# Optimization experiments

Measured on AMD Instinct MI355X. Metric: run time of the kernel, lower is better.

## Reference

```python
import jax, jax.numpy as jnp
import numpy as np

EPS = 1e-5

def _bin(t):
    # sign() with straight-through estimator (matches the .data-mutation trick)
    s = jnp.where(t >= 0, 1.0, -1.0).astype(t.dtype)
    return t + jax.lax.stop_gradient(s - t)

def _bn(x, g, b, m, v):
    # BatchNorm1d in eval mode: running mean/var
    return (x - m) * (g * jax.lax.rsqrt(v + EPS)) + b

def _hardtanh(x):
    return jnp.clip(x, -1.0, 1.0)

def setup_inputs() -> dict:
    key = jax.random.key(0)
    ks = jax.random.split(key, 24)
    B, D, H, C = 16384, 784, 768, 10
    d = {}
    d["x"] = jax.random.normal(ks[0], (B, D), jnp.float32)
    # BinarizeLinear weights (will be sign-binarized in forward) + real-valued biases
    d["W1"] = jax.random.normal(ks[1], (H, D), jnp.float32) * 0.05
    d["b1"] = jax.random.normal(ks[2], (H,), jnp.float32) * 0.05
    d["W2"] = jax.random.normal(ks[3], (H, H), jnp.float32) * 0.05
    d["b2"] = jax.random.normal(ks[4], (H,), jnp.float32) * 0.05
    d["W3"] = jax.random.normal(ks[5], (H, H), jnp.float32) * 0.05
    d["b3"] = jax.random.normal(ks[6], (H,), jnp.float32) * 0.05
    d["W4"] = jax.random.normal(ks[7], (C, H), jnp.float32) * 0.05
    d["b4"] = jax.random.normal(ks[8], (C,), jnp.float32) * 0.05
    # BatchNorm params (eval-mode running stats)
    for i, kk in zip((1, 2, 3), ((9, 10, 11, 12), (13, 14, 15, 16), (17, 18, 19, 20))):
        d[f"g{i}"] = jax.random.normal(ks[kk[0]], (H,), jnp.float32) * 0.1 + 1.0
        d[f"be{i}"] = jax.random.normal(ks[kk[1]], (H,), jnp.float32) * 0.1
        d[f"m{i}"] = jax.random.normal(ks[kk[2]], (H,), jnp.float32) * 0.1
        d[f"v{i}"] = jax.random.uniform(ks[kk[3]], (H,), jnp.float32, 0.5, 1.5)
    return d

def reference(x, W1, b1, W2, b2, W3, b3, W4, b4,
              g1, be1, m1, v1, g2, be2, m2, v2, g3, be3, m3, v3):
    x = x.reshape(-1, 784)
    # fc1: input has 784 features -> input NOT binarized; weight binarized
    h = x @ _bin(W1).T + b1
    h = _hardtanh(_bn(h, g1, be1, m1, v1))
    # fc2: input binarized, weight binarized
    h = _bin(h) @ _bin(W2).T + b2
    h = _hardtanh(_bn(h, g2, be2, m2, v2))
    # fc3 (dropout is identity in eval mode)
    h = _bin(h) @ _bin(W3).T + b3
    h = _hardtanh(_bn(h, g3, be3, m3, v3))
    # fc4: plain Linear + LogSoftmax
    logits = h @ W4.T + b4
    return jax.nn.log_softmax(logits, axis=-1)
```

## Files before the change

### kernel.cpp

```cpp
#include <hip/hip_runtime.h>
#include <math.h>
#include <stdint.h>

#define NB 16384
#define NH 768
#define ND 784
#define NC 10
#define NW 12

__global__ void k_bnprep_f32(const float* __restrict__ g, const float* __restrict__ be,
                             const float* __restrict__ m, const float* __restrict__ v,
                             const float* __restrict__ bias, float* __restrict__ out) {
    int i = blockIdx.x * 256 + threadIdx.x;
    if (i >= NH) return;
    float t1 = __fadd_rn(v[i], 1e-5f);
    float t2 = __fsqrt_rn(t1);
    float t3 = __fdiv_rn(1.0f, t2);
    out[i]          = __fmul_rn(g[i], t3);
    out[NH + i]     = m[i];
    out[2 * NH + i] = be[i];
    out[3 * NH + i] = bias[i];
}

__global__ void k_pack_w1bf(const float* __restrict__ W1, unsigned short* __restrict__ wbf) {
    int k = blockIdx.x * 256 + threadIdx.x;
    int col = blockIdx.y;
    if (k >= ND) return;
    float v = W1[(size_t)col * ND + k];
    wbf[(size_t)col * ND + k] = (v >= 0.0f) ? (unsigned short)0x3F80 : (unsigned short)0xBF80;
}

__global__ void k_pack_wT(const float* __restrict__ W, unsigned long long* __restrict__ wT) {
    int idx = blockIdx.x * 256 + threadIdx.x;
    if (idx >= NH * NW) return;
    int col = idx / NW, j = idx % NW;
    unsigned long long w = 0ull;
    for (int l = 0; l < 64; ++l) {
        float v = W[(size_t)col * NH + j * 64 + l];
        w |= (unsigned long long)(v >= 0.0f ? 1 : 0) << l;
    }
    wT[(size_t)j * NH + col] = w;
}

__global__ __launch_bounds__(512, 4)
void k_gemm1_bf(const float* __restrict__ x, const unsigned short* __restrict__ wbf,
                const float* __restrict__ bnp,
                unsigned int* __restrict__ s1p32) {
    __shared__ float xs[8][ND];
    __shared__ alignas(16) unsigned short wl[32][808];
    const int tid = threadIdx.x;
    const int r0 = blockIdx.x * 8;
    const int wave = tid >> 6, lane = tid & 63;
    const int colsub = lane & 31, jh = lane >> 5;
    const int j0 = jh * 8;

    {
        const float4* src = (const float4*)(x + (size_t)(r0 + wave) * ND);
        float4* dst = (float4*)&xs[wave][0];
        for (int k4 = lane; k4 < 196; k4 += 64) dst[k4] = src[k4];
    }

    const float* xrow = &xs[wave][j0];

#pragma unroll 1
    for (int tile = 0; tile < 2; ++tile) {
        const int c0 = blockIdx.y * 64 + tile * 32;
        __syncthreads();
        {
            int c = tid >> 4, q = tid & 15;
            uint4* dst = (uint4*)&wl[c][0];
            const uint4* srcp = (const uint4*)(wbf + (size_t)(c0 + c) * ND);
#pragma unroll
            for (int k4 = q; k4 < 98; k4 += 16) dst[k4] = srcp[k4];
        }
        __syncthreads();

        const unsigned short* wrow = &wl[colsub][j0];

        float a[4][8];
#pragma unroll
        for (int g = 0; g < 4; ++g)
#pragma unroll
            for (int i = 0; i < 8; ++i) a[g][i] = 0.0f;

#pragma unroll
        for (int t = 0; t < 12; ++t) {
#pragma unroll
            for (int g = 0; g < 4; ++g) {
                const int kk = t * 64 + g * 16;
                uint4 wA = *(const uint4*)(wrow + kk);
                float4 x0 = *(const float4*)(xrow + kk);
                float4 x1 = *(const float4*)(xrow + kk + 4);
                unsigned int dw[4] = {wA.x, wA.y, wA.z, wA.w};
                float wf[8];
#pragma unroll
                for (int p = 0; p < 4; ++p) {
                    wf[2 * p]     = __uint_as_float(dw[p] << 16);
                    wf[2 * p + 1] = __uint_as_float(dw[p] & 0xFFFF0000u);
                }
                float xv[8] = {x0.x, x0.y, x0.z, x0.w, x1.x, x1.y, x1.z, x1.w};
#pragma unroll
                for (int i = 0; i < 8; ++i)
                    a[g][i] = __fmaf_rn(wf[i], xv[i], a[g][i]);
            }
        }
        {
            const int kk = 768;
            uint4 wA = *(const uint4*)(wrow + kk);
            float4 x0 = *(const float4*)(xrow + kk);
            float4 x1 = *(const float4*)(xrow + kk + 4);
            unsigned int dw[4] = {wA.x, wA.y, wA.z, wA.w};
            float wf[8];
#pragma unroll
            for (int p = 0; p < 4; ++p) {
                wf[2 * p]     = __uint_as_float(dw[p] << 16);
                wf[2 * p + 1] = __uint_as_float(dw[p] & 0xFFFF0000u);
            }
            float xv[8] = {x0.x, x0.y, x0.z, x0.w, x1.x, x1.y, x1.z, x1.w};
#pragma unroll
            for (int i = 0; i < 8; ++i)
                a[0][i] = __fmaf_rn(wf[i], xv[i], a[0][i]);
        }

        float v[8];
#pragma unroll
        for (int i = 0; i < 8; ++i)
            v[i] = __fadd_rn(__fadd_rn(a[0][i], a[1][i]), __fadd_rn(a[2][i], a[3][i]));
        float h8[8];
#pragma unroll
        for (int i = 0; i < 8; ++i) {
            float other = __shfl_xor(v[i], 32, 64);
            h8[i] = __fadd_rn(v[i], other);
        }
        float h4[4], h2[2];
#pragma unroll
        for (int i = 0; i < 4; ++i) h4[i] = __fadd_rn(h8[i], h8[i + 4]);
#pragma unroll
        for (int i = 0; i < 2; ++i) h2[i] = __fadd_rn(h4[i], h4[i + 2]);
        float acc = __fadd_rn(h2[0], h2[1]);

        const int col = c0 + colsub;
        const float sc = bnp[col], mm = bnp[NH + col], be = bnp[2 * NH + col],
                    bias = bnp[3 * NH + col];
        float h  = __fadd_rn(acc, bias);
        float t1 = __fsub_rn(h, mm);
        float u  = __fmul_rn(t1, sc);
        float hb = __fadd_rn(u, be);
        unsigned long long word = __ballot(hb >= 0.0f);
        if (lane == 0)
            s1p32[(size_t)(r0 + wave) * (2 * NW) + blockIdx.y * 2 + tile] =
                (unsigned int)word;
    }
}

template <int MODE>
__global__ __launch_bounds__(256, 2)
void k_popbin(const unsigned long long* __restrict__ Ap,
              const unsigned long long* __restrict__ wT,
              const float* __restrict__ bnp,
              unsigned long long* __restrict__ Sp, float* __restrict__ h_out) {
    __shared__ unsigned long long as[64][NW];
    const int tid = threadIdx.x;
    const int b0 = blockIdx.x * 64;

    {
        unsigned long long* asf = &as[0][0];
        const unsigned long long* src = Ap + (size_t)b0 * NW;
        for (int i = tid; i < 64 * NW; i += 256) asf[i] = src[i];
    }
    __syncthreads();

    const int wave = tid >> 6, lane = tid & 63;

    for (int chunk = 0; chunk < NW; ++chunk) {
        const int col = chunk * 64 + lane;
        unsigned long long w[NW];
#pragma unroll
        for (int j = 0; j < NW; ++j) w[j] = wT[(size_t)j * NH + col];
        const float sc = bnp[col], mm = bnp[NH + col], be = bnp[2 * NH + col],
                    bias = bnp[3 * NH + col];
        for (int r = 0; r < 16; ++r) {
            const int row = wave * 16 + r;
            int d = 0;
#pragma unroll
            for (int j = 0; j < NW; ++j)
                d += __builtin_popcountll(as[row][j] ^ w[j]);
            int dot = NH - 2 * d;
            float h  = __fadd_rn((float)dot, bias);
            float t  = __fsub_rn(h, mm);
            float u  = __fmul_rn(t, sc);
            float hb = __fadd_rn(u, be);
            if (MODE == 0) {
                unsigned long long word = __ballot(hb >= 0.0f);
                if (lane == 0) Sp[(size_t)(b0 + row) * NW + chunk] = word;
            } else {
                float hc = fminf(fmaxf(hb, -1.0f), 1.0f);
                h_out[(size_t)(b0 + row) * NH + col] = hc;
            }
        }
    }
}

__global__ __launch_bounds__(256, 4)
void k_fc4(const float* __restrict__ h3, const float* __restrict__ W4,
           const float* __restrict__ b4, float* __restrict__ out) {
    __shared__ float w4s[NC * NH];
    const int tid = threadIdx.x;
    for (int i = tid; i < NC * NH; i += 256) w4s[i] = W4[i];
    __syncthreads();

    const int wave = tid >> 6, lane = tid & 63;
    const int row = blockIdx.x * 4 + wave;
    const float* hrow = h3 + (size_t)row * NH;

    double p[NC];
#pragma unroll
    for (int c = 0; c < NC; ++c) p[c] = 0.0;

    for (int it = 0; it < NH / 64; ++it) {
        int j = it * 64 + lane;
        double hv = (double)hrow[j];
#pragma unroll
        for (int c = 0; c < NC; ++c) p[c] += hv * (double)w4s[c * NH + j];
    }
#pragma unroll
    for (int c = 0; c < NC; ++c) {
#pragma unroll
        for (int off = 32; off > 0; off >>= 1) p[c] += __shfl_xor(p[c], off, 64);
    }
    double lg[NC];
    double mx = -1e300;
#pragma unroll
    for (int c = 0; c < NC; ++c) {
        lg[c] = p[c] + (double)b4[c];
        mx = fmax(mx, lg[c]);
    }
    double s = 0.0;
#pragma unroll
    for (int c = 0; c < NC; ++c) s += exp(lg[c] - mx);
    double lse = mx + log(s);
    if (lane < NC) {
        double v = 0.0;
#pragma unroll
        for (int c = 0; c < NC; ++c)
            if (lane == c) v = lg[c];
        out[(size_t)row * NC + lane] = (float)(v - lse);
    }
}

extern "C" void kernel_launch(void* const* d_in, const int* in_sizes, int n_in,
                              void* d_out, int out_size, void* d_ws, size_t ws_size,
                              hipStream_t stream) {
    const float* x  = (const float*)d_in[0];
    const float* W1 = (const float*)d_in[1];
    const float* b1 = (const float*)d_in[2];
    const float* W2 = (const float*)d_in[3];
    const float* b2 = (const float*)d_in[4];
    const float* W3 = (const float*)d_in[5];
    const float* b3 = (const float*)d_in[6];
    const float* W4 = (const float*)d_in[7];
    const float* b4 = (const float*)d_in[8];
    const float* g1 = (const float*)d_in[9],  *be1 = (const float*)d_in[10];
    const float* m1 = (const float*)d_in[11], *v1  = (const float*)d_in[12];
    const float* g2 = (const float*)d_in[13], *be2 = (const float*)d_in[14];
    const float* m2 = (const float*)d_in[15], *v2  = (const float*)d_in[16];
    const float* g3 = (const float*)d_in[17], *be3 = (const float*)d_in[18];
    const float* m3 = (const float*)d_in[19], *v3  = (const float*)d_in[20];
    float* out = (float*)d_out;

    char* ws = (char*)d_ws;
    size_t off = 0;
    unsigned short* wbf = (unsigned short*)(ws + off);  off += (size_t)NH * ND * 2;
    unsigned long long* w2pT = (unsigned long long*)(ws + off); off += (size_t)NW * NH * 8;
    unsigned long long* w3pT = (unsigned long long*)(ws + off); off += (size_t)NW * NH * 8;
    unsigned long long* s1p  = (unsigned long long*)(ws + off); off += (size_t)NB * NW * 8;
    unsigned long long* s2p  = (unsigned long long*)(ws + off); off += (size_t)NB * NW * 8;
    float*  h3   = (float*)(ws + off);              off += (size_t)NB * NH * 4;
    float* bnp1 = (float*)(ws + off);               off += (size_t)4 * NH * 4;
    float* bnp2 = (float*)(ws + off);               off += (size_t)4 * NH * 4;
    float* bnp3 = (float*)(ws + off);               off += (size_t)4 * NH * 4;
    (void)ws_size; (void)in_sizes; (void)n_in; (void)out_size;

    k_pack_w1bf<<<dim3(4, NH), 256, 0, stream>>>(W1, wbf);
    k_pack_wT<<<dim3((NH * NW + 255) / 256), 256, 0, stream>>>(W2, w2pT);
    k_pack_wT<<<dim3((NH * NW + 255) / 256), 256, 0, stream>>>(W3, w3pT);
    k_bnprep_f32<<<dim3(3), 256, 0, stream>>>(g1, be1, m1, v1, b1, bnp1);
    k_bnprep_f32<<<dim3(3), 256, 0, stream>>>(g2, be2, m2, v2, b2, bnp2);
    k_bnprep_f32<<<dim3(3), 256, 0, stream>>>(g3, be3, m3, v3, b3, bnp3);

    k_gemm1_bf<<<dim3(NB / 8, NH / 64), 512, 0, stream>>>(x, wbf, bnp1,
                                                          (unsigned int*)s1p);
    k_popbin<0><<<dim3(NB / 64), 256, 0, stream>>>(s1p, w2pT, bnp2, s2p, nullptr);
    k_popbin<1><<<dim3(NB / 64), 256, 0, stream>>>(s2p, w3pT, bnp3, nullptr, h3);
    k_fc4<<<dim3(NB / 4), 256, 0, stream>>>(h3, W4, b4, out);
}
```

Baseline: 883.1 us.

## Use packed FP32 FMA and compute two rows per wave in gemm1

Rewrites the first-layer kernel so each wave handles two batch rows instead of one. This halves the block to 256 threads and reuses each decoded bf16 weight pair across both rows. The inner products use inline v_pk_fma_f32, doing two FMAs per instruction and cutting the VALU instruction count and LDS weight reads per output. The cost is more accumulator registers (64 floats) and fewer threads per block for the weight tile loads, which may lower occupancy.

```diff
diff --git a/kernel.cpp b/kernel.cpp
--- a/kernel.cpp
+++ b/kernel.cpp
@@ -7,6 +7,13 @@
 #define ND 784
 #define NC 10
 #define NW 12
+
+typedef float v2f __attribute__((ext_vector_type(2)));
+
+__device__ __forceinline__ v2f pkfma(v2f s0, v2f s1, v2f s2) {
+    asm("v_pk_fma_f32 %0, %1, %2, %0" : "+v"(s2) : "v"(s0), "v"(s1));
+    return s2;
+}
 
 __global__ void k_bnprep_f32(const float* __restrict__ g, const float* __restrict__ be,
                              const float* __restrict__ m, const float* __restrict__ v,
@@ -42,46 +49,50 @@
     wT[(size_t)j * NH + col] = w;
 }
 
-__global__ __launch_bounds__(512, 4)
-void k_gemm1_bf(const float* __restrict__ x, const unsigned short* __restrict__ wbf,
-                const float* __restrict__ bnp,
-                unsigned int* __restrict__ s1p32) {
+__global__ __launch_bounds__(256, 2)
+void k_gemm1_pk(const float* __restrict__ x, const unsigned short* __restrict__ wbf,
+                const float* __restrict__ bnp, unsigned int* __restrict__ s1p32) {
     __shared__ float xs[8][ND];
     __shared__ alignas(16) unsigned short wl[32][808];
+
     const int tid = threadIdx.x;
-    const int r0 = blockIdx.x * 8;
     const int wave = tid >> 6, lane = tid & 63;
     const int colsub = lane & 31, jh = lane >> 5;
     const int j0 = jh * 8;
+    const int rA = 2 * wave;
+    const int r0 = blockIdx.x * 8;
 
     {
-        const float4* src = (const float4*)(x + (size_t)(r0 + wave) * ND);
-        float4* dst = (float4*)&xs[wave][0];
-        for (int k4 = lane; k4 < 196; k4 += 64) dst[k4] = src[k4];
-    }
-
-    const float* xrow = &xs[wave][j0];
+        const float4* s0 = (const float4*)(x + (size_t)(r0 + rA) * ND);
+        const float4* s1 = (const float4*)(x + (size_t)(r0 + rA + 1) * ND);
+        float4* d0 = (float4*)&xs[rA][0];
+        float4* d1 = (float4*)&xs[rA + 1][0];
+        for (int k4 = lane; k4 < 196; k4 += 64) d0[k4] = s0[k4];
+        for (int k4 = lane; k4 < 196; k4 += 64) d1[k4] = s1[k4];
+    }
+
+    const float* xr0 = &xs[rA][j0];
+    const float* xr1 = &xs[rA + 1][j0];
 
 #pragma unroll 1
     for (int tile = 0; tile < 2; ++tile) {
         const int c0 = blockIdx.y * 64 + tile * 32;
         __syncthreads();
         {
-            int c = tid >> 4, q = tid & 15;
+            int c = tid >> 3, q0 = tid & 7;
             uint4* dst = (uint4*)&wl[c][0];
             const uint4* srcp = (const uint4*)(wbf + (size_t)(c0 + c) * ND);
-#pragma unroll
-            for (int k4 = q; k4 < 98; k4 += 16) dst[k4] = srcp[k4];
+            for (int q = q0; q < 98; q += 8) dst[q] = srcp[q];
         }
         __syncthreads();
 
         const unsigned short* wrow = &wl[colsub][j0];
 
-        float a[4][8];
+        v2f a0[4][4], a1[4][4];
 #pragma unroll
         for (int g = 0; g < 4; ++g)
 #pragma unroll
-            for (int i = 0; i < 8; ++i) a[g][i] = 0.0f;
+            for (int p = 0; p < 4; ++p) { a0[g][p] = (v2f){0.f, 0.f}; a1[g][p] = (v2f){0.f, 0.f}; }
 
 #pragma unroll
         for (int t = 0; t < 12; ++t) {
@@ -89,67 +100,90 @@
             for (int g = 0; g < 4; ++g) {
                 const int kk = t * 64 + g * 16;
                 uint4 wA = *(const uint4*)(wrow + kk);
-                float4 x0 = *(const float4*)(xrow + kk);
-                float4 x1 = *(const float4*)(xrow + kk + 4);
+                float4 x0 = *(const float4*)(xr0 + kk);
+                float4 x1 = *(const float4*)(xr0 + kk + 4);
+                float4 y0 = *(const float4*)(xr1 + kk);
+                float4 y1 = *(const float4*)(xr1 + kk + 4);
                 unsigned int dw[4] = {wA.x, wA.y, wA.z, wA.w};
-                float wf[8];
+                v2f wp[4];
 #pragma unroll
                 for (int p = 0; p < 4; ++p) {
-                    wf[2 * p]     = __uint_as_float(dw[p] << 16);
-                    wf[2 * p + 1] = __uint_as_float(dw[p] & 0xFFFF0000u);
+                    wp[p].x = __uint_as_float(dw[p] << 16);
+                    wp[p].y = __uint_as_float(dw[p] & 0xFFFF0000u);
                 }
-                float xv[8] = {x0.x, x0.y, x0.z, x0.w, x1.x, x1.y, x1.z, x1.w};
-#pragma unroll
-                for (int i = 0; i < 8; ++i)
-                    a[g][i] = __fmaf_rn(wf[i], xv[i], a[g][i]);
+                a0[g][0] = pkfma(wp[0], (v2f){x0.x, x0.y}, a0[g][0]);
+                a0[g][1] = pkfma(wp[1], (v2f){x0.z, x0.w}, a0[g][1]);
+                a0[g][2] = pkfma(wp[2], (v2f){x1.x, x1.y}, a0[g][2]);
+                a0[g][3] = pkfma(wp[3], (v2f){x1.z, x1.w}, a0[g][3]);
+                a1[g][0] = pkfma(wp[0], (v2f){y0.x, y0.y}, a1[g][0]);
+                a1[g][1] = pkfma(wp[1], (v2f){y0.z, y0.w}, a1[g][1]);
+                a1[g][2] = pkfma(wp[2], (v2f){y1.x, y1.y}, a1[g][2]);
+                a1[g][3] = pkfma(wp[3], (v2f){y1.z, y1.w}, a1[g][3]);
             }
         }
         {
             const int kk = 768;
             uint4 wA = *(const uint4*)(wrow + kk);
-            float4 x0 = *(const float4*)(xrow + kk);
-            float4 x1 = *(const float4*)(xrow + kk + 4);
+            float4 x0 = *(const float4*)(xr0 + kk);
+            float4 x1 = *(const float4*)(xr0 + kk + 4);
+            float4 y0 = *(const float4*)(xr1 + kk);
+            float4 y1 = *(const float4*)(xr1 + kk + 4);
             unsigned int dw[4] = {wA.x, wA.y, wA.z, wA.w};
-            float wf[8];
+            v2f wp[4];
 #pragma unroll
             for (int p = 0; p < 4; ++p) {
-                wf[2 * p]     = __uint_as_float(dw[p] << 16);
-                wf[2 * p + 1] = __uint_as_float(dw[p] & 0xFFFF0000u);
+                wp[p].x = __uint_as_float(dw[p] << 16);
+                wp[p].y = __uint_as_float(dw[p] & 0xFFFF0000u);
             }
-            float xv[8] = {x0.x, x0.y, x0.z, x0.w, x1.x, x1.y, x1.z, x1.w};
-#pragma unroll
-            for (int i = 0; i < 8; ++i)
-                a[0][i] = __fmaf_rn(wf[i], xv[i], a[0][i]);
-        }
-
-        float v[8];
-#pragma unroll
-        for (int i = 0; i < 8; ++i)
-            v[i] = __fadd_rn(__fadd_rn(a[0][i], a[1][i]), __fadd_rn(a[2][i], a[3][i]));
-        float h8[8];
-#pragma unroll
-        for (int i = 0; i < 8; ++i) {
-            float other = __shfl_xor(v[i], 32, 64);
-            h8[i] = __fadd_rn(v[i], other);
-        }
-        float h4[4], h2[2];
-#pragma unroll
-        for (int i = 0; i < 4; ++i) h4[i] = __fadd_rn(h8[i], h8[i + 4]);
-#pragma unroll
-        for (int i = 0; i < 2; ++i) h2[i] = __fadd_rn(h4[i], h4[i + 2]);
-        float acc = __fadd_rn(h2[0], h2[1]);
+            a0[0][0] = pkfma(wp[0], (v2f){x0.x, x0.y}, a0[0][0]);
+            a0[0][1] = pkfma(wp[1], (v2f){x0.z, x0.w}, a0[0][1]);
+            a0[0][2] = pkfma(wp[2], (v2f){x1.x, x1.y}, a0[0][2]);
+            a0[0][3] = pkfma(wp[3], (v2f){x1.z, x1.w}, a0[0][3]);
+            a1[0][0] = pkfma(wp[0], (v2f){y0.x, y0.y}, a1[0][0]);
+            a1[0][1] = pkfma(wp[1], (v2f){y0.z, y0.w}, a1[0][1]);
+            a1[0][2] = pkfma(wp[2], (v2f){y1.x, y1.y}, a1[0][2]);
+            a1[0][3] = pkfma(wp[3], (v2f){y1.z, y1.w}, a1[0][3]);
+        }
 
         const int col = c0 + colsub;
         const float sc = bnp[col], mm = bnp[NH + col], be = bnp[2 * NH + col],
                     bias = bnp[3 * NH + col];
-        float h  = __fadd_rn(acc, bias);
-        float t1 = __fsub_rn(h, mm);
-        float u  = __fmul_rn(t1, sc);
-        float hb = __fadd_rn(u, be);
-        unsigned long long word = __ballot(hb >= 0.0f);
-        if (lane == 0)
-            s1p32[(size_t)(r0 + wave) * (2 * NW) + blockIdx.y * 2 + tile] =
-                (unsigned int)word;
+
+#define COMB_EPI_PK(A, RIDX)                                                   \
+        {                                                                      \
+            float v_[8];                                                       \
+            _Pragma("unroll")                                                  \
+            for (int p = 0; p < 4; ++p) {                                      \
+                v_[2 * p] = __fadd_rn(__fadd_rn(A[0][p].x, A[1][p].x),         \
+                                      __fadd_rn(A[2][p].x, A[3][p].x));        \
+                v_[2 * p + 1] = __fadd_rn(__fadd_rn(A[0][p].y, A[1][p].y),     \
+                                          __fadd_rn(A[2][p].y, A[3][p].y));    \
+            }                                                                  \
+            float h8[8];                                                       \
+            _Pragma("unroll")                                                  \
+            for (int i = 0; i < 8; ++i) {                                      \
+                float o = __shfl_xor(v_[i], 32, 64);                           \
+                h8[i] = __fadd_rn(v_[i], o);                                   \
+            }                                                                  \
+            float h4[4], h2[2];                                                \
+            _Pragma("unroll")                                                  \
+            for (int i = 0; i < 4; ++i) h4[i] = __fadd_rn(h8[i], h8[i + 4]);   \
+            _Pragma("unroll")                                                  \
+            for (int i = 0; i < 2; ++i) h2[i] = __fadd_rn(h4[i], h4[i + 2]);   \
+            float acc = __fadd_rn(h2[0], h2[1]);                               \
+            float h  = __fadd_rn(acc, bias);                                   \
+            float t1 = __fsub_rn(h, mm);                                       \
+            float u  = __fmul_rn(t1, sc);                                      \
+            float hb = __fadd_rn(u, be);                                       \
+            unsigned long long word = __ballot(hb >= 0.0f);                    \
+            if (lane == 0)                                                     \
+                s1p32[(size_t)(r0 + rA + (RIDX)) * (2 * NW) +                  \
+                      blockIdx.y * 2 + tile] = (unsigned int)word;             \
+        }
+
+        COMB_EPI_PK(a0, 0)
+        COMB_EPI_PK(a1, 1)
+#undef COMB_EPI_PK
     }
 }
 
@@ -288,7 +322,7 @@
     k_bnprep_f32<<<dim3(3), 256, 0, stream>>>(g2, be2, m2, v2, b2, bnp2);
     k_bnprep_f32<<<dim3(3), 256, 0, stream>>>(g3, be3, m3, v3, b3, bnp3);
 
-    k_gemm1_bf<<<dim3(NB / 8, NH / 64), 512, 0, stream>>>(x, wbf, bnp1,
+    k_gemm1_pk<<<dim3(NB / 8, NH / 64), 256, 0, stream>>>(x, wbf, bnp1,
                                                           (unsigned int*)s1p);
     k_popbin<0><<<dim3(NB / 64), 256, 0, stream>>>(s1p, w2pT, bnp2, s2p, nullptr);
     k_popbin<1><<<dim3(NB / 64), 256, 0, stream>>>(s2p, w3pT, bnp3, nullptr, h3);
```

Measured after the change: 960.9 us. 8.8% more time.
